# Kernel optimization log

Hardware: AMD Instinct MI355X
Metric: run time of the kernel (lower is better)

The kernel has to match this reference:

```python
import jax, jax.numpy as jnp
import numpy as np

BETA = 1.0
GAMMA = 0.25


def setup_inputs() -> dict:
    key = jax.random.key(0)
    ks = jax.random.split(key, 8)
    N, D_in, D_h, D_z = 65536, 1024, 512, 256
    s = lambda fan_in: 1.0 / np.sqrt(fan_in)
    return {
        "x": jax.random.normal(ks[0], (N, D_in), jnp.float32),
        "eW1": jax.random.normal(ks[1], (D_in, D_h), jnp.float32) * s(D_in),
        "eb1": jnp.zeros((D_h,), jnp.float32),
        "eW2": jax.random.normal(ks[2], (D_h, D_z), jnp.float32) * s(D_h),
        "eb2": jnp.zeros((D_z,), jnp.float32),
        "dW1": jax.random.normal(ks[3], (D_z, D_h), jnp.float32) * s(D_z),
        "db1": jnp.zeros((D_h,), jnp.float32),
        "dW2": jax.random.normal(ks[4], (D_h, D_in), jnp.float32) * s(D_h),
        "db2": jnp.zeros((D_in,), jnp.float32),
        "C0": jax.random.normal(ks[5], (1024, D_z), jnp.float32),
        "C1": jax.random.normal(ks[6], (512, D_z), jnp.float32),
        "C2": jax.random.normal(ks[7], (256, D_z), jnp.float32),
    }


def _nearest_idx(r, C):
    # argmin of squared euclidean distance == argmin of cdist(p=2)
    r = jax.lax.stop_gradient(r)
    d2 = jnp.sum(r * r, -1, keepdims=True) - 2.0 * (r @ C.T) + jnp.sum(C * C, -1)
    return jnp.argmin(d2, axis=-1)


def reference(x, eW1, eb1, eW2, eb2, dW1, db1, dW2, db2, C0, C1, C2):
    sg = jax.lax.stop_gradient
    # encoder: Linear -> GELU (exact) -> Linear
    z = jax.nn.gelu(x @ eW1 + eb1, approximate=False) @ eW2 + eb2
    residual = z
    output = jnp.zeros_like(z)
    losses = []
    for C in (C0, C1, C2):
        idx = _nearest_idx(residual, sg(C))
        q = C[idx]                                    # [N, 256] gather
        z2c = jnp.mean((residual - sg(q)) ** 2)       # commit input to code
        c2z = jnp.mean((sg(residual) - q) ** 2)       # move code to input
        losses.append(BETA * c2z + GAMMA * z2c)
        output = output + q
        residual = residual - q
    # straight-through: z + sg(zq) - sg(z)
    h = z + sg(output) - sg(z)
    out = jax.nn.gelu(h @ dW1 + db1, approximate=False) @ dW2 + db2
    recon_loss = jnp.mean((out - x) ** 2)
    return jnp.stack([recon_loss] + losses)  # [4]: recon, commit0, commit1, commit2
```

## Files before the change

kernel.cpp:

```cpp
#include <hip/hip_runtime.h>
#include <cstddef>


typedef __attribute__((ext_vector_type(8))) __bf16 bf16x8;
typedef __attribute__((ext_vector_type(4))) float f32x4;
typedef unsigned short u16;

__device__ __forceinline__ u16 f2bf(float f) {
    unsigned u = __float_as_uint(f);
    u += 0x7fffu + ((u >> 16) & 1u);
    return (u16)(u >> 16);
}
__device__ __forceinline__ float gelu_exact(float v) {
    return 0.5f * v * (1.0f + erff(v * 0.7071067811865475f));
}
__device__ __forceinline__ void gload16(const void* g, void* l) {
    __builtin_amdgcn_global_load_lds(
        (const __attribute__((address_space(1))) void*)g,
        (__attribute__((address_space(3))) void*)l, 16, 0, 0);
}
__device__ __forceinline__ f32x4 mfma_bf16(bf16x8 a, bf16x8 b, f32x4 c) {
    return __builtin_amdgcn_mfma_f32_16x16x32_bf16(a, b, c, 0, 0, 0);
}

__global__ __launch_bounds__(256)
void prep_weights(const float* __restrict__ eW1, const float* __restrict__ eW2,
                  const float* __restrict__ dW1, const float* __restrict__ dW2,
                  u16* __restrict__ eW1t, u16* __restrict__ eW2t,
                  u16* __restrict__ dW1t, u16* __restrict__ dW2t)
{
    const int b = blockIdx.x, t = threadIdx.x;
    if (b < 2048) {
        int e = b * 256 + t;
        int n = e >> 10, k = e & 1023;
        eW1t[e] = f2bf(eW1[(size_t)k * 512 + n]);
    } else if (b < 2560) {
        int e = (b - 2048) * 256 + t;
        int n = e >> 9, k = e & 511;
        eW2t[e] = f2bf(eW2[(size_t)k * 256 + n]);
    } else if (b < 3072) {
        int e = (b - 2560) * 256 + t;
        int n = e >> 8, k = e & 255;
        dW1t[e] = f2bf(dW1[(size_t)k * 512 + n]);
    } else {
        int e = (b - 3072) * 256 + t;
        int n = e >> 9, k = e & 511;
        dW2t[e] = f2bf(dW2[(size_t)k * 1024 + n]);
    }
}

__global__ __launch_bounds__(256)
void cb_prep(const float* __restrict__ C0, const float* __restrict__ C1,
             const float* __restrict__ C2, u16* __restrict__ Cbf,
             float* __restrict__ cnorm)
{
    __shared__ float red[256];
    const int code = blockIdx.x, t = threadIdx.x;
    const float* C;
    int local;
    if (code < 1024)      { C = C0; local = code; }
    else if (code < 1536) { C = C1; local = code - 1024; }
    else                  { C = C2; local = code - 1536; }
    const float v = C[(size_t)local * 256 + t];
    Cbf[(size_t)code * 256 + t] = f2bf(v);
    red[t] = v * v;
    __syncthreads();
    for (int s = 128; s; s >>= 1) { if (t < s) red[t] += red[t + s]; __syncthreads(); }
    if (t == 0) cnorm[code] = red[0];
}

template <int EPI, bool AF32>
__global__ __launch_bounds__(256, 2)
void gemm_mfma(const void* __restrict__ Aptr, const u16* __restrict__ Bt,
               const float* __restrict__ bias, u16* __restrict__ Obf,
               float* __restrict__ Of, const float* __restrict__ X,
               float* __restrict__ lossOut, int N, int K, int ntn,
               float lossScale)
{
    __shared__ __align__(16) u16 As[2][128 * 32];
    __shared__ __align__(16) u16 Bs[2][128 * 32];

    const int nwg = gridDim.x;
    const int bid = blockIdx.x;
    const int wg  = (bid & 7) * (nwg >> 3) + (bid >> 3);
    const int brow = (wg / ntn) * 128;
    const int bcol = (wg % ntn) * 128;

    const int t    = threadIdx.x;
    const int lane = t & 63;
    const int wid  = t >> 6;
    const int wrow = (wid >> 1) * 64, wcol = (wid & 1) * 64;
    const int lrow = lane & 15, lk8 = (lane >> 4) * 8;

    const int nt = K >> 5;

    f32x4 acc[4][4];
#pragma unroll
    for (int m = 0; m < 4; ++m)
#pragma unroll
        for (int n = 0; n < 4; ++n) acc[m][n] = (f32x4)0.f;

    const u16*   Abf = (const u16*)Aptr;
    const float* Af  = (const float*)Aptr;

    auto stageB = [&](int kt, int buf) {
#pragma unroll
        for (int it = 0; it < 2; ++it) {
            const int e0 = (it * 256 + t) * 8;
            const int row = e0 >> 5, col = e0 & 31;
            gload16(&Bt[(size_t)(bcol + row) * K + kt * 32 + col],
                    (char*)&Bs[buf][0] + (size_t)e0 * 2);
        }
    };
    auto stageA_bf = [&](int kt, int buf) {
#pragma unroll
        for (int it = 0; it < 2; ++it) {
            const int e0 = (it * 256 + t) * 8;
            const int row = e0 >> 5, col = e0 & 31;
            gload16(&Abf[(size_t)(brow + row) * K + kt * 32 + col],
                    (char*)&As[buf][0] + (size_t)e0 * 2);
        }
    };
    auto issueA_f32 = [&](int kt, float4* r) {
#pragma unroll
        for (int it = 0; it < 4; ++it) {
            const int e0 = (it * 256 + t) * 4;
            const int row = e0 >> 5, col = e0 & 31;
            r[it] = *(const float4*)&Af[(size_t)(brow + row) * K + kt * 32 + col];
        }
    };
    auto writeA_f32 = [&](int buf, const float4* r) {
#pragma unroll
        for (int it = 0; it < 4; ++it) {
            const int e0 = (it * 256 + t) * 4;
            const float4 v = r[it];
            unsigned lo = (unsigned)f2bf(v.x) | ((unsigned)f2bf(v.y) << 16);
            unsigned hi = (unsigned)f2bf(v.z) | ((unsigned)f2bf(v.w) << 16);
            *(uint2*)((char*)&As[buf][0] + (size_t)e0 * 2) = make_uint2(lo, hi);
        }
    };

    if (AF32) {
        float4 r0[4];
        issueA_f32(0, r0);
        stageB(0, 0);
        writeA_f32(0, r0);
    } else {
        stageA_bf(0, 0);
        stageB(0, 0);
    }
    __syncthreads();

    int cur = 0;
    for (int kt = 0; kt < nt; ++kt) {
        const bool last = (kt == nt - 1);
        float4 rnext[4];
        if (!last) {
            if (AF32) issueA_f32(kt + 1, rnext);
            else      stageA_bf(kt + 1, cur ^ 1);
            stageB(kt + 1, cur ^ 1);
        }
        bf16x8 a[4], b[4];
#pragma unroll
        for (int m = 0; m < 4; ++m)
            a[m] = *(const bf16x8*)&As[cur][(wrow + m * 16 + lrow) * 32 + lk8];
#pragma unroll
        for (int n = 0; n < 4; ++n)
            b[n] = *(const bf16x8*)&Bs[cur][(wcol + n * 16 + lrow) * 32 + lk8];
#pragma unroll
        for (int m = 0; m < 4; ++m)
#pragma unroll
            for (int n = 0; n < 4; ++n)
                acc[m][n] = mfma_bf16(a[m], b[n], acc[m][n]);

        if (AF32 && !last) writeA_f32(cur ^ 1, rnext);
        __syncthreads();
        cur ^= 1;
    }

    int   colN[4];
    float bn[4];
#pragma unroll
    for (int n = 0; n < 4; ++n) {
        colN[n] = bcol + wcol + n * 16 + lrow;
        bn[n]   = bias[colN[n]];
    }

    if (EPI == 0) {
#pragma unroll
        for (int m = 0; m < 4; ++m) {
            const int rowb = brow + wrow + m * 16 + (lane >> 4) * 4;
#pragma unroll
            for (int n = 0; n < 4; ++n)
#pragma unroll
                for (int j = 0; j < 4; ++j)
                    Obf[(size_t)(rowb + j) * N + colN[n]] =
                        f2bf(gelu_exact(acc[m][n][j] + bn[n]));
        }
    } else if (EPI == 1) {
#pragma unroll
        for (int m = 0; m < 4; ++m) {
            const int rowb = brow + wrow + m * 16 + (lane >> 4) * 4;
#pragma unroll
            for (int n = 0; n < 4; ++n)
#pragma unroll
                for (int j = 0; j < 4; ++j)
                    Of[(size_t)(rowb + j) * N + colN[n]] = acc[m][n][j] + bn[n];
        }
    } else {
        float partial = 0.f;
#pragma unroll
        for (int m = 0; m < 4; ++m) {
            const int rowb = brow + wrow + m * 16 + (lane >> 4) * 4;
#pragma unroll
            for (int n = 0; n < 4; ++n)
#pragma unroll
                for (int j = 0; j < 4; ++j) {
                    const float o = acc[m][n][j] + bn[n];
                    const float d = o - X[(size_t)(rowb + j) * N + colN[n]];
                    partial = fmaf(d, d, partial);
                }
        }
        float* red = (float*)&As[0][0];
        red[t] = partial;
        __syncthreads();
        for (int s = 128; s; s >>= 1) { if (t < s) red[t] += red[t + s]; __syncthreads(); }
        if (t == 0) atomicAdd(lossOut, red[0] * lossScale);
    }
}

__global__ __launch_bounds__(256, 3)
void vq_mfma(const float* __restrict__ Z, const u16* __restrict__ Cbf,
             const float* __restrict__ cnorm,
             const float* __restrict__ C0, const float* __restrict__ C1,
             const float* __restrict__ C2,
             u16* __restrict__ ZQ, float* __restrict__ lossOut)
{
    __shared__ __align__(16) u16 Rb[64][264];
    __shared__ __align__(16) u16 Cs[2][4096];
    __shared__ int   idxs[3][64];
    __shared__ float lred[256];

    const int t    = threadIdx.x;
    const int lane = t & 63;
    const int wid  = t >> 6;
    const int lrow = lane & 15, g = lane >> 4;
    const int brow = blockIdx.x * 64;

    float R[64];
#pragma unroll
    for (int r = 0; r < 64; ++r) R[r] = Z[(size_t)(brow + r) * 256 + t];

    const float* Cf[3]  = {C0, C1, C2};
    const int ncodes[3] = {1024, 512, 256};
    const int coff[3]   = {0, 1024, 1536};
    const float lscale  = 1.25f / (65536.0f * 256.0f);

#pragma unroll
    for (int stage = 0; stage < 3; ++stage) {
        const u16*   Cb  = Cbf + (size_t)coff[stage] * 256;
        const float* cns = cnorm + coff[stage];
        const int ntiles = ncodes[stage] >> 5;

        auto stageC = [&](int tile, int kh, int buf) {
#pragma unroll
            for (int it = 0; it < 2; ++it) {
                const int d   = (it * 256 + t) * 16;
                const int row = d >> 8;
                const int kb  = d & 255;
                const int kbs = kb ^ ((row & 7) << 4);
                gload16(&Cb[(size_t)(tile * 32 + row) * 256 + kh * 128 + (kbs >> 1)],
                        (char*)&Cs[buf][0] + d);
            }
        };

        stageC(0, 0, 0);
#pragma unroll
        for (int r = 0; r < 64; ++r) Rb[r][t] = f2bf(R[r]);
        __syncthreads();

        bf16x8 a[8];
#pragma unroll
        for (int ks = 0; ks < 8; ++ks)
            a[ks] = *(const bf16x8*)&Rb[wid * 16 + lrow][ks * 32 + g * 8];

        float best[4]; int bidx[4];
#pragma unroll
        for (int j = 0; j < 4; ++j) { best[j] = 3.0e38f; bidx[j] = 0; }

#pragma unroll 1
        for (int tile = 0; tile < ntiles; ++tile) {
            f32x4 acc[2];
            acc[0] = (f32x4)0.f; acc[1] = (f32x4)0.f;

            stageC(tile, 1, 1);
            const float cn0 = cns[tile * 32 + lrow];
            const float cn1 = cns[tile * 32 + 16 + lrow];
#pragma unroll
            for (int ks2 = 0; ks2 < 4; ++ks2)
#pragma unroll
                for (int n = 0; n < 2; ++n) {
                    const int row = n * 16 + lrow;
                    const int kb2 = ks2 * 64 + g * 16;
                    bf16x8 b = *(const bf16x8*)((const char*)&Cs[0][0]
                                 + row * 256 + (kb2 ^ ((row & 7) << 4)));
                    acc[n] = mfma_bf16(a[ks2], b, acc[n]);
                }
            __syncthreads();

            if (tile + 1 < ntiles) stageC(tile + 1, 0, 0);
#pragma unroll
            for (int ks2 = 0; ks2 < 4; ++ks2)
#pragma unroll
                for (int n = 0; n < 2; ++n) {
                    const int row = n * 16 + lrow;
                    const int kb2 = ks2 * 64 + g * 16;
                    bf16x8 b = *(const bf16x8*)((const char*)&Cs[1][0]
                                 + row * 256 + (kb2 ^ ((row & 7) << 4)));
                    acc[n] = mfma_bf16(a[4 + ks2], b, acc[n]);
                }
#pragma unroll
            for (int n = 0; n < 2; ++n) {
                const int code = tile * 32 + n * 16 + lrow;
                const float cn = n ? cn1 : cn0;
#pragma unroll
                for (int j = 0; j < 4; ++j) {
                    const float s = fmaf(-2.0f, acc[n][j], cn);
                    if (s < best[j]) { best[j] = s; bidx[j] = code; }
                }
            }
            __syncthreads();
        }

#pragma unroll
        for (int j = 0; j < 4; ++j) {
            float v = best[j]; int i = bidx[j];
#pragma unroll
            for (int d = 1; d < 16; d <<= 1) {
                const float ov = __shfl_xor(v, d);
                const int   oi = __shfl_xor(i, d);
                if (ov < v || (ov == v && oi < i)) { v = ov; i = oi; }
            }
            if (lrow == 0) idxs[stage][wid * 16 + g * 4 + j] = i;
        }
        __syncthreads();

        const float* Cfs = Cf[stage];
        float partial = 0.f;
#pragma unroll
        for (int r = 0; r < 64; ++r) {
            const float q  = Cfs[(size_t)idxs[stage][r] * 256 + t];
            const float rn = R[r] - q;
            R[r] = rn;
            partial = fmaf(rn, rn, partial);
        }
        lred[t] = partial;
        __syncthreads();
        for (int s = 128; s; s >>= 1) { if (t < s) lred[t] += lred[t + s]; __syncthreads(); }
        if (t == 0) atomicAdd(&lossOut[1 + stage], lred[0] * lscale);
        __syncthreads();
    }

#pragma unroll
    for (int r = 0; r < 64; ++r) {
        const float zq = C0[(size_t)idxs[0][r] * 256 + t]
                       + C1[(size_t)idxs[1][r] * 256 + t]
                       + C2[(size_t)idxs[2][r] * 256 + t];
        ZQ[(size_t)(brow + r) * 256 + t] = f2bf(zq);
    }
}

extern "C" void kernel_launch(void* const* d_in, const int* in_sizes, int n_in,
                              void* d_out, int out_size, void* d_ws, size_t ws_size,
                              hipStream_t stream)
{
    const float* x   = (const float*)d_in[0];
    const float* eW1 = (const float*)d_in[1];
    const float* eb1 = (const float*)d_in[2];
    const float* eW2 = (const float*)d_in[3];
    const float* eb2 = (const float*)d_in[4];
    const float* dW1 = (const float*)d_in[5];
    const float* db1 = (const float*)d_in[6];
    const float* dW2 = (const float*)d_in[7];
    const float* db2 = (const float*)d_in[8];
    const float* C0  = (const float*)d_in[9];
    const float* C1  = (const float*)d_in[10];
    const float* C2  = (const float*)d_in[11];
    float* out = (float*)d_out;

    char* w = (char*)d_ws;
    u16*   H1   = (u16*)(w);
    float* Zf   = (float*)(w + ((size_t)64 << 20));
    u16*   ZQ   = (u16*)(w + ((size_t)128 << 20));
    u16*   H2   = (u16*)(w + ((size_t)160 << 20));
    u16*   eW1t = (u16*)(w + ((size_t)224 << 20));
    u16*   eW2t = (u16*)(w + ((size_t)225 << 20));
    u16*   dW1t = (u16*)(w + ((size_t)226 << 20));
    u16*   dW2t = (u16*)(w + ((size_t)227 << 20));
    u16*   Cbf  = (u16*)(w + ((size_t)228 << 20));
    float* cn   = (float*)(w + ((size_t)229 << 20));

    hipMemsetAsync(d_out, 0, 4 * sizeof(float), stream);

    prep_weights<<<5120, 256, 0, stream>>>(eW1, eW2, dW1, dW2, eW1t, eW2t, dW1t, dW2t);
    cb_prep<<<1792, 256, 0, stream>>>(C0, C1, C2, Cbf, cn);

    gemm_mfma<0, true><<<2048, 256, 0, stream>>>(
        x, eW1t, eb1, H1, nullptr, nullptr, nullptr, 512, 1024, 4, 0.f);
    gemm_mfma<1, false><<<1024, 256, 0, stream>>>(
        H1, eW2t, eb2, nullptr, Zf, nullptr, nullptr, 256, 512, 2, 0.f);
    vq_mfma<<<1024, 256, 0, stream>>>(Zf, Cbf, cn, C0, C1, C2, ZQ, out);
    gemm_mfma<0, false><<<2048, 256, 0, stream>>>(
        ZQ, dW1t, db1, H2, nullptr, nullptr, nullptr, 512, 256, 4, 0.f);
    gemm_mfma<2, false><<<4096, 256, 0, stream>>>(
        H2, dW2t, db2, nullptr, nullptr, x, out, 1024, 512, 8,
        1.0f / (65536.0f * 1024.0f));
}
```

Measured before the change: 673.3 us.

## Split VQ codebook search across 8 waves with direct global codebook loads

The VQ kernel now runs 512 threads per block: four row groups times two code-column groups, with each thread holding half the residual rows. The LDS double-buffered codebook staging and its per-tile barriers are dropped; each wave reads bf16 codebook rows straight from global/L2 into MFMA operands. A cross-wave argmin merge through shared memory combines the two code halves. This aims to cut register pressure and barrier stalls and raise occupancy, at the cost of uncoalesced global codebook reads and no LDS reuse across waves.

New measurement: 831.2 us. 1.23x slower.

```diff
diff --git a/kernel.cpp b/kernel.cpp
--- a/kernel.cpp
+++ b/kernel.cpp
@@ -229,7 +229,7 @@
     }
 }
 
-__global__ __launch_bounds__(256, 3)
+__global__ __launch_bounds__(512, 4)
 void vq_mfma(const float* __restrict__ Z, const u16* __restrict__ Cbf,
              const float* __restrict__ cnorm,
              const float* __restrict__ C0, const float* __restrict__ C1,
@@ -237,99 +237,63 @@
              u16* __restrict__ ZQ, float* __restrict__ lossOut)
 {
     __shared__ __align__(16) u16 Rb[64][264];
-    __shared__ __align__(16) u16 Cs[2][4096];
+    __shared__ float redv[64][2];
+    __shared__ int   redi[64][2];
     __shared__ int   idxs[3][64];
-    __shared__ float lred[256];
+    __shared__ float lred[512];
 
     const int t    = threadIdx.x;
     const int lane = t & 63;
     const int wid  = t >> 6;
+    const int rg   = wid & 3;
+    const int cg   = wid >> 2;
     const int lrow = lane & 15, g = lane >> 4;
+    const int col  = t & 255;
+    const int rh   = t >> 8;
     const int brow = blockIdx.x * 64;
 
-    float R[64];
-#pragma unroll
-    for (int r = 0; r < 64; ++r) R[r] = Z[(size_t)(brow + r) * 256 + t];
+    float R[32];
+#pragma unroll
+    for (int r = 0; r < 32; ++r)
+        R[r] = Z[(size_t)(brow + rh * 32 + r) * 256 + col];
 
     const float* Cf[3]  = {C0, C1, C2};
     const int ncodes[3] = {1024, 512, 256};
     const int coff[3]   = {0, 1024, 1536};
     const float lscale  = 1.25f / (65536.0f * 256.0f);
 
-#pragma unroll
     for (int stage = 0; stage < 3; ++stage) {
+#pragma unroll
+        for (int r = 0; r < 32; ++r) Rb[rh * 32 + r][col] = f2bf(R[r]);
+        __syncthreads();
+
+        bf16x8 a[8];
+#pragma unroll
+        for (int ks = 0; ks < 8; ++ks)
+            a[ks] = *(const bf16x8*)&Rb[rg * 16 + lrow][ks * 32 + g * 8];
+
+        float best[4]; int bidx[4];
+#pragma unroll
+        for (int j = 0; j < 4; ++j) { best[j] = 3.0e38f; bidx[j] = 0; }
+
         const u16*   Cb  = Cbf + (size_t)coff[stage] * 256;
         const float* cns = cnorm + coff[stage];
-        const int ntiles = ncodes[stage] >> 5;
-
-        auto stageC = [&](int tile, int kh, int buf) {
-#pragma unroll
-            for (int it = 0; it < 2; ++it) {
-                const int d   = (it * 256 + t) * 16;
-                const int row = d >> 8;
-                const int kb  = d & 255;
-                const int kbs = kb ^ ((row & 7) << 4);
-                gload16(&Cb[(size_t)(tile * 32 + row) * 256 + kh * 128 + (kbs >> 1)],
-                        (char*)&Cs[buf][0] + d);
+        const int nch = ncodes[stage] >> 5;
+
+#pragma unroll 2
+        for (int ch = 0; ch < nch; ++ch) {
+            const int code = ch * 32 + cg * 16 + lrow;
+            const float cn = cns[code];
+            const u16* bp = &Cb[(size_t)code * 256 + g * 8];
+            f32x4 acc = (f32x4)0.f;
+#pragma unroll
+            for (int ks = 0; ks < 8; ++ks)
+                acc = mfma_bf16(a[ks], *(const bf16x8*)&bp[ks * 32], acc);
+#pragma unroll
+            for (int j = 0; j < 4; ++j) {
+                const float s = fmaf(-2.0f, acc[j], cn);
+                if (s < best[j]) { best[j] = s; bidx[j] = code; }
             }
-        };
-
-        stageC(0, 0, 0);
-#pragma unroll
-        for (int r = 0; r < 64; ++r) Rb[r][t] = f2bf(R[r]);
-        __syncthreads();
-
-        bf16x8 a[8];
-#pragma unroll
-        for (int ks = 0; ks < 8; ++ks)
-            a[ks] = *(const bf16x8*)&Rb[wid * 16 + lrow][ks * 32 + g * 8];
-
-        float best[4]; int bidx[4];
-#pragma unroll
-        for (int j = 0; j < 4; ++j) { best[j] = 3.0e38f; bidx[j] = 0; }
-
-#pragma unroll 1
-        for (int tile = 0; tile < ntiles; ++tile) {
-            f32x4 acc[2];
-            acc[0] = (f32x4)0.f; acc[1] = (f32x4)0.f;
-
-            stageC(tile, 1, 1);
-            const float cn0 = cns[tile * 32 + lrow];
-            const float cn1 = cns[tile * 32 + 16 + lrow];
-#pragma unroll
-            for (int ks2 = 0; ks2 < 4; ++ks2)
-#pragma unroll
-                for (int n = 0; n < 2; ++n) {
-                    const int row = n * 16 + lrow;
-                    const int kb2 = ks2 * 64 + g * 16;
-                    bf16x8 b = *(const bf16x8*)((const char*)&Cs[0][0]
-                                 + row * 256 + (kb2 ^ ((row & 7) << 4)));
-                    acc[n] = mfma_bf16(a[ks2], b, acc[n]);
-                }
-            __syncthreads();
-
-            if (tile + 1 < ntiles) stageC(tile + 1, 0, 0);
-#pragma unroll
-            for (int ks2 = 0; ks2 < 4; ++ks2)
-#pragma unroll
-                for (int n = 0; n < 2; ++n) {
-                    const int row = n * 16 + lrow;
-                    const int kb2 = ks2 * 64 + g * 16;
-                    bf16x8 b = *(const bf16x8*)((const char*)&Cs[1][0]
-                                 + row * 256 + (kb2 ^ ((row & 7) << 4)));
-                    acc[n] = mfma_bf16(a[4 + ks2], b, acc[n]);
-                }
-#pragma unroll
-            for (int n = 0; n < 2; ++n) {
-                const int code = tile * 32 + n * 16 + lrow;
-                const float cn = n ? cn1 : cn0;
-#pragma unroll
-                for (int j = 0; j < 4; ++j) {
-                    const float s = fmaf(-2.0f, acc[n][j], cn);
-                    if (s < best[j]) { best[j] = s; bidx[j] = code; }
-                }
-            }
-            __syncthreads();
         }
 
 #pragma unroll
@@ -341,32 +305,43 @@
                 const int   oi = __shfl_xor(i, d);
                 if (ov < v || (ov == v && oi < i)) { v = ov; i = oi; }
             }
-            if (lrow == 0) idxs[stage][wid * 16 + g * 4 + j] = i;
+            if (lrow == 0) {
+                redv[rg * 16 + g * 4 + j][cg] = v;
+                redi[rg * 16 + g * 4 + j][cg] = i;
+            }
+        }
+        __syncthreads();
+        if (t < 64) {
+            float v = redv[t][0]; int i = redi[t][0];
+            const float ov = redv[t][1]; const int oi = redi[t][1];
+            if (ov < v || (ov == v && oi < i)) { v = ov; i = oi; }
+            idxs[stage][t] = i;
         }
         __syncthreads();
 
         const float* Cfs = Cf[stage];
         float partial = 0.f;
 #pragma unroll
-        for (int r = 0; r < 64; ++r) {
-            const float q  = Cfs[(size_t)idxs[stage][r] * 256 + t];
+        for (int r = 0; r < 32; ++r) {
+            const float q  = Cfs[(size_t)idxs[stage][rh * 32 + r] * 256 + col];
             const float rn = R[r] - q;
             R[r] = rn;
             partial = fmaf(rn, rn, partial);
         }
         lred[t] = partial;
         __syncthreads();
-        for (int s = 128; s; s >>= 1) { if (t < s) lred[t] += lred[t + s]; __syncthreads(); }
+        for (int s = 256; s; s >>= 1) { if (t < s) lred[t] += lred[t + s]; __syncthreads(); }
         if (t == 0) atomicAdd(&lossOut[1 + stage], lred[0] * lscale);
         __syncthreads();
     }
 
 #pragma unroll
-    for (int r = 0; r < 64; ++r) {
-        const float zq = C0[(size_t)idxs[0][r] * 256 + t]
-                       + C1[(size_t)idxs[1][r] * 256 + t]
-                       + C2[(size_t)idxs[2][r] * 256 + t];
-        ZQ[(size_t)(brow + r) * 256 + t] = f2bf(zq);
+    for (int r = 0; r < 32; ++r) {
+        const int row = rh * 32 + r;
+        const float zq = C0[(size_t)idxs[0][row] * 256 + col]
+                       + C1[(size_t)idxs[1][row] * 256 + col]
+                       + C2[(size_t)idxs[2][row] * 256 + col];
+        ZQ[(size_t)(brow + row) * 256 + col] = f2bf(zq);
     }
 }
 
@@ -409,7 +384,7 @@
         x, eW1t, eb1, H1, nullptr, nullptr, nullptr, 512, 1024, 4, 0.f);
     gemm_mfma<1, false><<<1024, 256, 0, stream>>>(
         H1, eW2t, eb2, nullptr, Zf, nullptr, nullptr, 256, 512, 2, 0.f);
-    vq_mfma<<<1024, 256, 0, stream>>>(Zf, Cbf, cn, C0, C1, C2, ZQ, out);
+    vq_mfma<<<1024, 512, 0, stream>>>(Zf, Cbf, cn, C0, C1, C2, ZQ, out);
     gemm_mfma<0, false><<<2048, 256, 0, stream>>>(
         ZQ, dW1t, db1, H2, nullptr, nullptr, nullptr, 512, 256, 4, 0.f);
     gemm_mfma<2, false><<<4096, 256, 0, stream>>>(
```
